# Kernel optimization log

Measured on AMD Instinct MI355X. Metric: run time of the kernel, lower is better.

The kernel has to match this reference:

```python
import jax, jax.numpy as jnp
import numpy as np

SIGMA = 1.0
DELTA = 1.0
TOPK = 10
TOPK_HALF = 5  # int(np.around(TOPK / 2))
N, D = 4096, 512
N_IDS = 2048  # N / view


def _l2_normalize(x, eps=1e-12):
    n = jnp.linalg.norm(x, axis=1, keepdims=True)
    return x / jnp.maximum(n, eps)


def _cdist(a, b):
    # Euclidean distance with a sqrt that is safe at 0 (diagonal).
    sq = (jnp.sum(a * a, 1)[:, None] + jnp.sum(b * b, 1)[None, :]
          - 2.0 * (a @ b.T))
    sq = jnp.maximum(sq, 0.0)
    return jnp.where(sq > 0, jnp.sqrt(jnp.where(sq > 0, sq, 1.0)), 0.0)


def setup_inputs() -> dict:
    key = jax.random.key(0)
    k1, k2, k3 = jax.random.split(key, 3)
    s_emb = jax.random.normal(k1, (N, D), dtype=jnp.float32)
    t_emb = jax.random.normal(k2, (N, D), dtype=jnp.float32)
    idx = jax.random.randint(k3, (N,), 0, N_IDS, dtype=jnp.int64)
    return {"s_emb": s_emb, "t_emb": t_emb, "idx": idx}


def reference(s_emb, t_emb, idx):
    n = s_emb.shape[0]
    s = _l2_normalize(s_emb)          # disable_mu=True
    t = _l2_normalize(t_emb)

    S_dist = _cdist(s, s)
    S_dist = S_dist / jnp.mean(S_dist, axis=1, keepdims=True)

    # --- teacher-side neighbor graph (no_grad in original) ---
    T_dist = _cdist(t, t)
    W_P = jnp.exp(-(T_dist ** 2) / SIGMA)                      # [N,N]
    same = idx[:, None] == idx[None, :]
    W_P_copy = jnp.where(same, 1.0, W_P)
    _, topk_index = jax.lax.top_k(W_P_copy, TOPK)              # [N,k]
    topk_half_index = topk_index[:, :TOPK_HALF]                # [N,k/2]

    rows = jnp.arange(n)[:, None]
    W_NN = jnp.zeros((n, n), jnp.float32).at[rows, topk_index].set(1.0)
    V = ((W_NN + W_NN.T) / 2.0 == 1.0).astype(jnp.float32)     # mutual kNN

    # Vectorized form of the per-row nonzero gather-reduce loop:
    # W_C_tilda[i,j] = V[i,j] * (sum_l V[i,l] V[j,l]) / |{l: V[i,l]>0}|
    row_cnt = jnp.sum(V, axis=1)                               # [N]
    VV = jnp.einsum('il,jl->ij', V, V)                         # [N,N]
    W_C_tilda = jnp.where(V > 0, VV / jnp.maximum(row_cnt, 1.0)[:, None], 0.0)

    W_C_hat = jnp.mean(W_C_tilda[topk_half_index], axis=1)     # [N,k/2,N]->[N,N]
    W_C = (W_C_hat + W_C_hat.T) / 2.0
    W = (W_P + W_C) / 2.0

    eye = jnp.eye(n, dtype=jnp.float32)
    pos_weight = W * (1.0 - eye)
    neg_weight = (1.0 - W) * (1.0 - eye)

    pull = jnp.maximum(S_dist, 0.0) ** 2 * pos_weight
    push = jnp.maximum(DELTA - S_dist, 0.0) ** 2 * neg_weight
    loss = (jnp.sum(pull) + jnp.sum(push)) / (n * (n - 1))
    return loss
```

## Files before the change

### kernel.cpp

```cpp
#include <hip/hip_runtime.h>
#include <math.h>

#define N 4096
#define D 512
#define TOPK 10
#define TOPK_HALF 5
#define NT 32
#define TRI_BLOCKS (NT * (NT + 1) / 2)
#define WC_BLOCKS (N * TOPK_HALF / 16)
#define INV_N (1.0f / 4096.0f)
#define TPAD 132

typedef __bf16 bf16;
typedef __bf16 bf16x8 __attribute__((ext_vector_type(8)));
typedef float f32x4 __attribute__((ext_vector_type(4)));
typedef _Float16 f16;
typedef _Float16 f16x4 __attribute__((ext_vector_type(4)));
typedef _Float16 f16x8 __attribute__((ext_vector_type(8)));
typedef unsigned short u16;
typedef unsigned short u16x8 __attribute__((ext_vector_type(8)));
typedef unsigned int u32;

__device__ __forceinline__ void gl_lds16(const void* g, void* l) {
  __builtin_amdgcn_global_load_lds(
      (const __attribute__((address_space(1))) void*)g,
      (__attribute__((address_space(3))) void*)l, 16, 0, 0);
}

__device__ __forceinline__ float f16tof(u16 h) {
  return (float)__builtin_bit_cast(_Float16, h);
}

__global__ __launch_bounds__(256) void k_normalize2(const float* __restrict__ xs,
                                                    const float* __restrict__ xt,
                                                    bf16* __restrict__ ys,
                                                    bf16* __restrict__ yt,
                                                    float* __restrict__ rsq_s,
                                                    float* __restrict__ rsq_t,
                                                    float* __restrict__ rowsum) {
  int b = blockIdx.x;
  int row = b & (N - 1);
  int is_t = b >> 12;
  const float* x = is_t ? xt : xs;
  bf16* y = is_t ? yt : ys;
  float* rowsq = is_t ? rsq_t : rsq_s;
  int tid = threadIdx.x;
  const float* xr = x + (size_t)row * D;
  float v0 = xr[tid], v1 = xr[tid + 256];
  float ss = v0 * v0 + v1 * v1;
  __shared__ float red[4];
  for (int off = 32; off > 0; off >>= 1) ss += __shfl_down(ss, off, 64);
  if ((tid & 63) == 0) red[tid >> 6] = ss;
  __syncthreads();
  float tot = red[0] + red[1] + red[2] + red[3];
  float inv = 1.0f / fmaxf(sqrtf(tot), 1e-12f);
  bf16 b0 = (bf16)(v0 * inv), b1 = (bf16)(v1 * inv);
  bf16* yr = y + (size_t)row * D;
  yr[tid] = b0; yr[tid + 256] = b1;
  float f0 = (float)b0, f1 = (float)b1;
  float s2 = f0 * f0 + f1 * f1;
  for (int off = 32; off > 0; off >>= 1) s2 += __shfl_down(s2, off, 64);
  __syncthreads();
  if ((tid & 63) == 0) red[tid >> 6] = s2;
  __syncthreads();
  if (tid == 0) {
    rowsq[row] = red[0] + red[1] + red[2] + red[3];
    if (!is_t) rowsum[row] = 0.f;
  }
}

__global__ __launch_bounds__(256) void k_dgram3(const bf16* __restrict__ S,
                                                const bf16* __restrict__ T,
                                                const float* __restrict__ rsq_s,
                                                const float* __restrict__ rsq_t,
                                                f16* __restrict__ Gsd,
                                                f16* __restrict__ Gwp,
                                                float* __restrict__ rowsum) {
  __shared__ __align__(16) char sm[128 * TPAD * 2];
  bf16* Jb0 = (bf16*)sm;
  bf16* Jb1 = (bf16*)(sm + 8192);
  bf16* Ib0 = (bf16*)(sm + 16384);
  bf16* Ib1 = (bf16*)(sm + 24576);
  f16* tp = (f16*)sm;

  int z = blockIdx.y;
  const bf16* Y = z ? T : S;
  const float* rsq = z ? rsq_t : rsq_s;
  f16* G = z ? Gwp : Gsd;

  int t = blockIdx.x, by = 0;
  while (t >= NT - by) { t -= NT - by; ++by; }
  int bx = by + t;
  bool offdiag = (bx != by);

  int tid = threadIdx.x;
  int lane = tid & 63, w = tid >> 6;
  int wr = w >> 1, wc = w & 1;
  int quad = lane >> 4, c = lane & 15;

  const char* Jbase = (const char*)(Y + (size_t)(bx * 128) * D);
  const char* Ibase = (const char*)(Y + (size_t)(by * 128) * D);
  int r0 = tid >> 2, q0 = tid & 3;
  int r1 = (tid + 256) >> 2, q1 = (tid + 256) & 3;
  size_t so0 = (size_t)r0 * (D * 2) + q0 * 16;
  size_t so1 = (size_t)r1 * (D * 2) + q1 * 16;
  bf16* lJ0a = Jb0 + (size_t)w * 512;  bf16* lJ0b = Jb0 + (size_t)(256 + w * 64) * 8;
  bf16* lJ1a = Jb1 + (size_t)w * 512;  bf16* lJ1b = Jb1 + (size_t)(256 + w * 64) * 8;
  bf16* lI0a = Ib0 + (size_t)w * 512;  bf16* lI0b = Ib0 + (size_t)(256 + w * 64) * 8;
  bf16* lI1a = Ib1 + (size_t)w * 512;  bf16* lI1b = Ib1 + (size_t)(256 + w * 64) * 8;

  int jrow = wr * 64 + c;
  int irow = wc * 64 + c;
  int kq = quad * 8;

  f32x4 acc[4][4] = {};
  for (int k0 = 0; k0 < D; k0 += 64) {
    size_t kb = (size_t)k0 * 2;
    gl_lds16(Jbase + so0 + kb,      lJ0a);
    gl_lds16(Jbase + so1 + kb,      lJ0b);
    gl_lds16(Jbase + so0 + kb + 64, lJ1a);
    gl_lds16(Jbase + so1 + kb + 64, lJ1b);
    gl_lds16(Ibase + so0 + kb,      lI0a);
    gl_lds16(Ibase + so1 + kb,      lI0b);
    gl_lds16(Ibase + so0 + kb + 64, lI1a);
    gl_lds16(Ibase + so1 + kb + 64, lI1b);
    __syncthreads();
    {
      bf16x8 af[4], bfr[4];
#pragma unroll
      for (int u = 0; u < 4; ++u) af[u] = *(bf16x8*)&Jb0[(jrow + u * 16) * 32 + kq];
#pragma unroll
      for (int v = 0; v < 4; ++v) bfr[v] = *(bf16x8*)&Ib0[(irow + v * 16) * 32 + kq];
#pragma unroll
      for (int u = 0; u < 4; ++u)
#pragma unroll
        for (int v = 0; v < 4; ++v)
          acc[u][v] = __builtin_amdgcn_mfma_f32_16x16x32_bf16(af[u], bfr[v], acc[u][v], 0, 0, 0);
    }
    {
      bf16x8 af[4], bfr[4];
#pragma unroll
      for (int u = 0; u < 4; ++u) af[u] = *(bf16x8*)&Jb1[(jrow + u * 16) * 32 + kq];
#pragma unroll
      for (int v = 0; v < 4; ++v) bfr[v] = *(bf16x8*)&Ib1[(irow + v * 16) * 32 + kq];
#pragma unroll
      for (int u = 0; u < 4; ++u)
#pragma unroll
        for (int v = 0; v < 4; ++v)
          acc[u][v] = __builtin_amdgcn_mfma_f32_16x16x32_bf16(af[u], bfr[v], acc[u][v], 0, 0, 0);
    }
    __syncthreads();
  }

#pragma unroll
  for (int v = 0; v < 4; ++v) {
    int il = wc * 64 + v * 16 + c;
    int ig = by * 128 + il;
    float ri = rsq[ig];
    float rsv = 0.f;
#pragma unroll
    for (int u = 0; u < 4; ++u) {
      int jl0 = wr * 64 + u * 16 + quad * 4;
      int jb0i = bx * 128 + jl0;
      float4 rj = *(const float4*)(rsq + jb0i);
      const float* rjp = (const float*)&rj;
      f32x4 a = acc[u][v];
      f16x4 st;
      if (z == 0) {
#pragma unroll
        for (int reg = 0; reg < 4; ++reg) {
          float sq = fmaxf(ri + rjp[reg] - 2.0f * a[reg], 0.0f);
          float val = sqrtf(sq);
          st[reg] = (_Float16)val;
          rsv += val;
        }
      } else {
#pragma unroll
        for (int reg = 0; reg < 4; ++reg) {
          float sq = fmaxf(ri + rjp[reg] - 2.0f * a[reg], 0.0f);
          st[reg] = (_Float16)expf(-sq);
        }
      }
      *(f16x4*)(G + (size_t)ig * N + jb0i) = st;
      if (offdiag) {
#pragma unroll
        for (int reg = 0; reg < 4; ++reg) tp[(jl0 + reg) * TPAD + il] = st[reg];
      }
    }
    if (z == 0) {
      rsv += __shfl_xor(rsv, 16, 64);
      rsv += __shfl_xor(rsv, 32, 64);
      if (lane < 16) atomicAdd(&rowsum[ig], rsv);
    }
  }

  if (offdiag) {
    __syncthreads();
    int rloc = tid >> 4;
    int cseg = tid & 15;
#pragma unroll
    for (int it = 0; it < 8; ++it) {
      int jl = it * 16 + rloc;
      int jg = bx * 128 + jl;
      f16x8 v8 = *(f16x8*)&tp[jl * TPAD + cseg * 8];
      *(f16x8*)(G + (size_t)jg * N + by * 128 + cseg * 8) = v8;
      if (z == 0) {
        float csum = 0.f;
#pragma unroll
        for (int e = 0; e < 8; ++e) csum += (float)v8[e];
        csum += __shfl_xor(csum, 1, 64);
        csum += __shfl_xor(csum, 2, 64);
        csum += __shfl_xor(csum, 4, 64);
        csum += __shfl_xor(csum, 8, 64);
        if (cseg == 0) atomicAdd(&rowsum[jg], csum);
      }
    }
  }
}

__global__ __launch_bounds__(256) void k_rowpass(const f16* __restrict__ Gs,
                                                 const f16* __restrict__ Gw,
                                                 const int* __restrict__ ids,
                                                 const float* __restrict__ rowsum,
                                                 int* __restrict__ topk,
                                                 double* __restrict__ pd) {
  __shared__ u32 lds[256 * TOPK];
  __shared__ double dred[4];
  int i = blockIdx.x, tid = threadIdx.x;
  int idi = ids[i];
  float invm = 1.0f / (rowsum[i] * INV_N);
  const u16* srow = (const u16*)(Gs + (size_t)i * N);
  const u16* wrow = (const u16*)(Gw + (size_t)i * N);
  u32 key[16];
  float dsum = 0.f;
  int j0 = tid * 16;
#pragma unroll
  for (int h = 0; h < 2; ++h) {
    int jb = j0 + h * 8;
    u16x8 sv = *(const u16x8*)(srow + jb);
    u16x8 wv = *(const u16x8*)(wrow + jb);
    int4 id0 = *(const int4*)(ids + jb);
    int4 id1 = *(const int4*)(ids + jb + 4);
    const int* idp = (const int*)&id0;
    const int* idp1 = (const int*)&id1;
#pragma unroll
    for (int e = 0; e < 8; ++e) {
      int j = jb + e;
      u16 hw = wv[e];
      float wp = f16tof(hw);
      if (j != i) {
        float sdn = f16tof(sv[e]) * invm;
        float r = fmaxf(1.0f - sdn, 0.0f); r *= r;
        dsum += r + 0.5f * wp * (sdn * sdn - r);
      }
      int idj = (e < 4) ? idp[e] : idp1[e - 4];
      u16 hk = (idj == idi) ? (u16)0x3C00 : hw;
      key[h * 8 + e] = ((u32)hk << 16) | (u32)(4095 - j);
    }
  }
#pragma unroll
  for (int kk = 2; kk <= 16; kk <<= 1) {
#pragma unroll
    for (int jj = kk >> 1; jj > 0; jj >>= 1) {
#pragma unroll
      for (int ii = 0; ii < 16; ++ii) {
        int ll = ii ^ jj;
        if (ll > ii) {
          bool desc = ((ii & kk) == 0);
          u32 a = key[ii], b = key[ll];
          bool sw = desc ? (a < b) : (a > b);
          key[ii] = sw ? b : a;
          key[ll] = sw ? a : b;
        }
      }
    }
  }
  double dl = (double)dsum;
  for (int off = 32; off > 0; off >>= 1) dl += __shfl_down(dl, off, 64);
  if ((tid & 63) == 0) dred[tid >> 6] = dl;
#pragma unroll
  for (int o = 0; o < TOPK; ++o) lds[tid * TOPK + o] = key[o];
  __syncthreads();
  for (int off = 128; off >= 1; off >>= 1) {
    if (tid < off) {
      u32 A[TOPK], B[TOPK];
#pragma unroll
      for (int o = 0; o < TOPK; ++o) {
        A[o] = lds[tid * TOPK + o];
        B[o] = lds[(tid + off) * TOPK + o];
      }
      u32 out[TOPK];
#pragma unroll
      for (int o = 0; o < TOPK; ++o) {
        u32 m = A[o] > B[o] ? A[o] : B[o];
#pragma unroll
        for (int p = 0; p < o; ++p) {
          u32 mn = A[p] < B[o - 1 - p] ? A[p] : B[o - 1 - p];
          m = m > mn ? m : mn;
        }
        out[o] = m;
      }
#pragma unroll
      for (int o = 0; o < TOPK; ++o) lds[tid * TOPK + o] = out[o];
    }
    __syncthreads();
  }
  if (tid == 0) {
#pragma unroll
    for (int o = 0; o < TOPK; ++o)
      topk[i * TOPK + o] = 4095 - (int)(lds[o] & 0xFFFu);
    pd[i] = dred[0] + dred[1] + dred[2] + dred[3];
  }
}

__global__ __launch_bounds__(64) void k_buildV(const int* __restrict__ topk,
                                               int* __restrict__ L,
                                               int* __restrict__ cnt) {
  int i = blockIdx.x * 64 + threadIdx.x;
  if (i >= N) return;
  int c = 0;
  for (int r = 0; r < TOPK; ++r) {
    int j = topk[i * TOPK + r];
    bool mut = false;
    for (int q = 0; q < TOPK; ++q) mut |= (topk[j * TOPK + q] == i);
    if (mut) L[i * TOPK + c++] = j;
  }
  cnt[i] = c;
}

__global__ __launch_bounds__(256) void k_wc(const int* __restrict__ topk,
                                            const int* __restrict__ L,
                                            const int* __restrict__ cnt,
                                            const f16* __restrict__ Gsd,
                                            const float* __restrict__ rowsum,
                                            double* __restrict__ pw) {
  __shared__ double red[16];
  int tid = threadIdx.x;
  int grp = tid >> 4;
  int gl = tid & 15;
  int task = blockIdx.x * 16 + grp;
  int i = task / TOPK_HALF, m = task % TOPK_HALF;
  int r = topk[i * TOPK + m];
  int cr = cnt[r];
  float invmi = 1.0f / (rowsum[i] * INV_N);
  int lval = (gl < cr) ? L[r * TOPK + gl] : -1;
  int Lr[TOPK];
#pragma unroll
  for (int a = 0; a < TOPK; ++a) Lr[a] = __shfl(lval, a, 16);
  float contrib = 0.f;
  if (gl < cr) {
    int j = lval;
    if (j != i) {
      int cj = cnt[j];
      float mj = rowsum[j] * INV_N;
      float sr_ = f16tof(((const u16*)Gsd)[(size_t)i * N + j]);
      int lj[TOPK];
#pragma unroll
      for (int b = 0; b < TOPK; ++b) lj[b] = L[j * TOPK + b];
      int vv = 0;
#pragma unroll
      for (int b = 0; b < TOPK; ++b) {
        if (b < cj) {
#pragma unroll
          for (int a = 0; a < TOPK; ++a)
            vv += ((a < cr) && (lj[b] == Lr[a])) ? 1 : 0;
        }
      }
      float denom = (float)(cr > 1 ? cr : 1);
      float wgt = (float)vv / denom;
      float sdij = sr_ * invmi;
      float sdji = sr_ / mj;
      float Rij = fmaxf(1.0f - sdij, 0.0f); Rij *= Rij;
      float Rji = fmaxf(1.0f - sdji, 0.0f); Rji *= Rji;
      float Fij = sdij * sdij - Rij;
      float Fji = sdji * sdji - Rji;
      contrib = wgt * (Fij + Fji);
    }
  }
  double local = (double)contrib;
  local += __shfl_xor(local, 1, 16);
  local += __shfl_xor(local, 2, 16);
  local += __shfl_xor(local, 4, 16);
  local += __shfl_xor(local, 8, 16);
  if (gl == 0) red[grp] = local;
  __syncthreads();
  if (tid == 0) {
    double s = 0.0;
#pragma unroll
    for (int g = 0; g < 16; ++g) s += red[g];
    pw[blockIdx.x] = s * (1.0 / 20.0);
  }
}

__global__ __launch_bounds__(256) void k_final(const double* __restrict__ pd,
                                               const double* __restrict__ pw,
                                               float* __restrict__ out) {
  int tid = threadIdx.x;
  double s = 0.0;
  for (int i = tid; i < N; i += 256) s += pd[i];
  for (int i = tid; i < WC_BLOCKS; i += 256) s += pw[i];
  for (int off = 32; off > 0; off >>= 1) s += __shfl_down(s, off, 64);
  __shared__ double red[4];
  if ((tid & 63) == 0) red[tid >> 6] = s;
  __syncthreads();
  if (tid == 0)
    out[0] = (float)((red[0] + red[1] + red[2] + red[3]) /
                     ((double)N * (double)(N - 1)));
}

extern "C" void kernel_launch(void* const* d_in, const int* in_sizes, int n_in,
                              void* d_out, int out_size, void* d_ws, size_t ws_size,
                              hipStream_t stream) {
  const float* s_emb = (const float*)d_in[0];
  const float* t_emb = (const float*)d_in[1];
  const int* ids = (const int*)d_in[2];
  float* out = (float*)d_out;

  char* ws = (char*)d_ws;
  size_t off = 0;
  bf16* snorm = (bf16*)(ws + off); off += (size_t)N * D * 2;
  bf16* tnorm = (bf16*)(ws + off); off += (size_t)N * D * 2;
  f16*  Gsd   = (f16*)(ws + off);  off += (size_t)N * N * 2;
  f16*  Gwp   = (f16*)(ws + off);  off += (size_t)N * N * 2;
  float* rsq_s = (float*)(ws + off); off += (size_t)N * 4;
  float* rsq_t = (float*)(ws + off); off += (size_t)N * 4;
  float* rowsum= (float*)(ws + off); off += (size_t)N * 4;
  int*   topk  = (int*)(ws + off);   off += (size_t)N * TOPK * 4;
  int*   L     = (int*)(ws + off);   off += (size_t)N * TOPK * 4;
  int*   cnt   = (int*)(ws + off);   off += (size_t)N * 4;
  off = (off + 15) & ~(size_t)15;
  double* pd   = (double*)(ws + off); off += (size_t)N * 8;
  double* pw   = (double*)(ws + off); off += (size_t)WC_BLOCKS * 8;

  k_normalize2<<<2 * N, 256, 0, stream>>>(s_emb, t_emb, snorm, tnorm,
                                          rsq_s, rsq_t, rowsum);
  k_dgram3<<<dim3(TRI_BLOCKS, 2), 256, 0, stream>>>(snorm, tnorm, rsq_s, rsq_t,
                                                    Gsd, Gwp, rowsum);
  k_rowpass<<<N, 256, 0, stream>>>(Gsd, Gwp, ids, rowsum, topk, pd);
  k_buildV<<<N / 64, 64, 0, stream>>>(topk, L, cnt);
  k_wc<<<WC_BLOCKS, 256, 0, stream>>>(topk, L, cnt, Gsd, rowsum, pw);
  k_final<<<1, 256, 0, stream>>>(pd, pw, out);
}
```

Before: 164.0 us.

## Double-buffer Gram tile loads, remap block order, use fast math, parallelize buildV

The Gram kernel now prefetches the next 32-wide K slice into a second LDS buffer while MFMAs consume the current one. It uses raw s_barrier and vmcnt waits instead of two __syncthreads per 64-wide step. Block indices are interleaved across the triangle so that heavy and light tiles spread more evenly. sqrt/exp switch to fast intrinsics, which may slightly change the rounding of the f16 outputs. k_buildV now gives each row a 16-lane group and compacts mutual neighbours with a ballot and popcount, replacing the serial per-thread loop.

```diff
diff --git a/kernel.cpp b/kernel.cpp
--- a/kernel.cpp
+++ b/kernel.cpp
@@ -77,10 +77,6 @@
                                                 f16* __restrict__ Gwp,
                                                 float* __restrict__ rowsum) {
   __shared__ __align__(16) char sm[128 * TPAD * 2];
-  bf16* Jb0 = (bf16*)sm;
-  bf16* Jb1 = (bf16*)(sm + 8192);
-  bf16* Ib0 = (bf16*)(sm + 16384);
-  bf16* Ib1 = (bf16*)(sm + 24576);
   f16* tp = (f16*)sm;
 
   int z = blockIdx.y;
@@ -88,7 +84,9 @@
   const float* rsq = z ? rsq_t : rsq_s;
   f16* G = z ? Gwp : Gsd;
 
-  int t = blockIdx.x, by = 0;
+  int orig = blockIdx.x;
+  int t = (orig & 7) * (TRI_BLOCKS / 8) + (orig >> 3);
+  int by = 0;
   while (t >= NT - by) { t -= NT - by; ++by; }
   int bx = by + t;
   bool offdiag = (bx != by);
@@ -97,6 +95,7 @@
   int lane = tid & 63, w = tid >> 6;
   int wr = w >> 1, wc = w & 1;
   int quad = lane >> 4, c = lane & 15;
+  int w1024 = w << 10;
 
   const char* Jbase = (const char*)(Y + (size_t)(bx * 128) * D);
   const char* Ibase = (const char*)(Y + (size_t)(by * 128) * D);
@@ -104,53 +103,54 @@
   int r1 = (tid + 256) >> 2, q1 = (tid + 256) & 3;
   size_t so0 = (size_t)r0 * (D * 2) + q0 * 16;
   size_t so1 = (size_t)r1 * (D * 2) + q1 * 16;
-  bf16* lJ0a = Jb0 + (size_t)w * 512;  bf16* lJ0b = Jb0 + (size_t)(256 + w * 64) * 8;
-  bf16* lJ1a = Jb1 + (size_t)w * 512;  bf16* lJ1b = Jb1 + (size_t)(256 + w * 64) * 8;
-  bf16* lI0a = Ib0 + (size_t)w * 512;  bf16* lI0b = Ib0 + (size_t)(256 + w * 64) * 8;
-  bf16* lI1a = Ib1 + (size_t)w * 512;  bf16* lI1b = Ib1 + (size_t)(256 + w * 64) * 8;
 
   int jrow = wr * 64 + c;
   int irow = wc * 64 + c;
   int kq = quad * 8;
 
+  char* bA = sm;
+  char* bB = sm + 16384;
+
+#define STAGE(buf, kb)                                   \
+  {                                                      \
+    char* _b = (buf);                                    \
+    gl_lds16(Jbase + so0 + (kb), _b + w1024);            \
+    gl_lds16(Jbase + so1 + (kb), _b + 4096 + w1024);     \
+    gl_lds16(Ibase + so0 + (kb), _b + 8192 + w1024);     \
+    gl_lds16(Ibase + so1 + (kb), _b + 12288 + w1024);    \
+  }
+
+#define COMPUTE(bufc)                                                          \
+  {                                                                            \
+    const bf16* Jc = (const bf16*)(bufc);                                      \
+    const bf16* Ic = (const bf16*)((bufc) + 8192);                             \
+    bf16x8 af[4], bfr[4];                                                      \
+    _Pragma("unroll") for (int u = 0; u < 4; ++u)                              \
+        af[u] = *(const bf16x8*)&Jc[(jrow + u * 16) * 32 + kq];                \
+    _Pragma("unroll") for (int v = 0; v < 4; ++v)                              \
+        bfr[v] = *(const bf16x8*)&Ic[(irow + v * 16) * 32 + kq];               \
+    _Pragma("unroll") for (int u = 0; u < 4; ++u)                              \
+      _Pragma("unroll") for (int v = 0; v < 4; ++v)                            \
+        acc[u][v] = __builtin_amdgcn_mfma_f32_16x16x32_bf16(                   \
+            af[u], bfr[v], acc[u][v], 0, 0, 0);                                \
+  }
+
   f32x4 acc[4][4] = {};
-  for (int k0 = 0; k0 < D; k0 += 64) {
-    size_t kb = (size_t)k0 * 2;
-    gl_lds16(Jbase + so0 + kb,      lJ0a);
-    gl_lds16(Jbase + so1 + kb,      lJ0b);
-    gl_lds16(Jbase + so0 + kb + 64, lJ1a);
-    gl_lds16(Jbase + so1 + kb + 64, lJ1b);
-    gl_lds16(Ibase + so0 + kb,      lI0a);
-    gl_lds16(Ibase + so1 + kb,      lI0b);
-    gl_lds16(Ibase + so0 + kb + 64, lI1a);
-    gl_lds16(Ibase + so1 + kb + 64, lI1b);
-    __syncthreads();
-    {
-      bf16x8 af[4], bfr[4];
-#pragma unroll
-      for (int u = 0; u < 4; ++u) af[u] = *(bf16x8*)&Jb0[(jrow + u * 16) * 32 + kq];
-#pragma unroll
-      for (int v = 0; v < 4; ++v) bfr[v] = *(bf16x8*)&Ib0[(irow + v * 16) * 32 + kq];
-#pragma unroll
-      for (int u = 0; u < 4; ++u)
-#pragma unroll
-        for (int v = 0; v < 4; ++v)
-          acc[u][v] = __builtin_amdgcn_mfma_f32_16x16x32_bf16(af[u], bfr[v], acc[u][v], 0, 0, 0);
-    }
-    {
-      bf16x8 af[4], bfr[4];
-#pragma unroll
-      for (int u = 0; u < 4; ++u) af[u] = *(bf16x8*)&Jb1[(jrow + u * 16) * 32 + kq];
-#pragma unroll
-      for (int v = 0; v < 4; ++v) bfr[v] = *(bf16x8*)&Ib1[(irow + v * 16) * 32 + kq];
-#pragma unroll
-      for (int u = 0; u < 4; ++u)
-#pragma unroll
-        for (int v = 0; v < 4; ++v)
-          acc[u][v] = __builtin_amdgcn_mfma_f32_16x16x32_bf16(af[u], bfr[v], acc[u][v], 0, 0, 0);
-    }
-    __syncthreads();
-  }
+  STAGE(bA, 0);
+  for (int tt = 0; tt < 15; ++tt) {
+    char* nb = (tt & 1) ? bA : bB;
+    char* cb = (tt & 1) ? bB : bA;
+    asm volatile("s_barrier" ::: "memory");
+    STAGE(nb, (size_t)(tt + 1) * 64);
+    asm volatile("s_waitcnt vmcnt(4)\n\ts_barrier" ::: "memory");
+    COMPUTE(cb);
+  }
+  asm volatile("s_waitcnt vmcnt(0)\n\ts_barrier" ::: "memory");
+  COMPUTE(bB);
+  __syncthreads();
+
+#undef STAGE
+#undef COMPUTE
 
 #pragma unroll
   for (int v = 0; v < 4; ++v) {
@@ -170,7 +170,7 @@
 #pragma unroll
         for (int reg = 0; reg < 4; ++reg) {
           float sq = fmaxf(ri + rjp[reg] - 2.0f * a[reg], 0.0f);
-          float val = sqrtf(sq);
+          float val = __builtin_amdgcn_sqrtf(sq);
           st[reg] = (_Float16)val;
           rsv += val;
         }
@@ -178,7 +178,7 @@
 #pragma unroll
         for (int reg = 0; reg < 4; ++reg) {
           float sq = fmaxf(ri + rjp[reg] - 2.0f * a[reg], 0.0f);
-          st[reg] = (_Float16)expf(-sq);
+          st[reg] = (_Float16)__expf(-sq);
         }
       }
       *(f16x4*)(G + (size_t)ig * N + jb0i) = st;
@@ -313,19 +313,25 @@
   }
 }
 
-__global__ __launch_bounds__(64) void k_buildV(const int* __restrict__ topk,
-                                               int* __restrict__ L,
-                                               int* __restrict__ cnt) {
-  int i = blockIdx.x * 64 + threadIdx.x;
-  if (i >= N) return;
-  int c = 0;
-  for (int r = 0; r < TOPK; ++r) {
-    int j = topk[i * TOPK + r];
-    bool mut = false;
+__global__ __launch_bounds__(256) void k_buildV(const int* __restrict__ topk,
+                                                int* __restrict__ L,
+                                                int* __restrict__ cnt) {
+  int tid = threadIdx.x;
+  int grp = tid >> 4, gl = tid & 15;
+  int i = blockIdx.x * 16 + grp;
+  bool act = (gl < TOPK);
+  int j = act ? topk[i * TOPK + gl] : 0;
+  bool mut = false;
+  if (act) {
+#pragma unroll
     for (int q = 0; q < TOPK; ++q) mut |= (topk[j * TOPK + q] == i);
-    if (mut) L[i * TOPK + c++] = j;
-  }
-  cnt[i] = c;
+  }
+  unsigned long long m = __ballot(mut);
+  int base = tid & 48;
+  unsigned gm = (unsigned)((m >> base) & 0xFFFFull);
+  int pos = __popc(gm & ((1u << gl) - 1));
+  if (mut) L[i * TOPK + pos] = j;
+  if (gl == 0) cnt[i] = __popc(gm);
 }
 
 __global__ __launch_bounds__(256) void k_wc(const int* __restrict__ topk,
@@ -437,7 +443,7 @@
   k_dgram3<<<dim3(TRI_BLOCKS, 2), 256, 0, stream>>>(snorm, tnorm, rsq_s, rsq_t,
                                                     Gsd, Gwp, rowsum);
   k_rowpass<<<N, 256, 0, stream>>>(Gsd, Gwp, ids, rowsum, topk, pd);
-  k_buildV<<<N / 64, 64, 0, stream>>>(topk, L, cnt);
+  k_buildV<<<N / 16, 256, 0, stream>>>(topk, L, cnt);
   k_wc<<<WC_BLOCKS, 256, 0, stream>>>(topk, L, cnt, Gsd, rowsum, pw);
   k_final<<<1, 256, 0, stream>>>(pd, pw, out);
 }
```

After: 146.9 us. -10.4%, faster.
